# Kernel optimization log

Measured on AMD Instinct MI355X. Metric: run time of the kernel, lower is better.

Reference implementation:

```python
import jax, jax.numpy as jnp
import numpy as np

DIM = 768
H = 12
HEAD = DIM // H
SCALE = HEAD ** -0.5
NMM, NV, NA = 8, 4, 4


def _cross_attn(x1, x2, qw, kvw, pw, pb):
    # x1: [B,N1,C] queries, x2: [B,N2,C] keys/values. Weights stored [in,out].
    B, N1, C = x1.shape
    N2 = x2.shape[1]
    q = (x1 @ qw).reshape(B, N1, H, HEAD).transpose(0, 2, 1, 3)        # [B,H,N1,d]
    kv = (x2 @ kvw).reshape(B, N2, 2, H, HEAD)
    k = kv[:, :, 0].transpose(0, 2, 1, 3)                               # [B,H,N2,d]
    v = kv[:, :, 1].transpose(0, 2, 1, 3)
    attn = jax.nn.softmax(jnp.einsum('bhnd,bhmd->bhnm', q, k) * SCALE, axis=-1)
    o = jnp.einsum('bhnm,bhmd->bhnd', attn, v).transpose(0, 2, 1, 3).reshape(B, N1, C)
    return o @ pw + pb, attn


def setup_inputs() -> dict:
    key = jax.random.key(0)
    ks = jax.random.split(key, 16)
    s = 0.02
    inp = {
        'xmm': jax.random.normal(ks[0], (64, 16, DIM), jnp.float32),
        'xv': jax.random.normal(ks[1], (64, 784, DIM), jnp.float32),
        'xa': jax.random.normal(ks[2], (64, 512, DIM), jnp.float32),
        # visual cross-attn params (weights stored [in,out] = torch W.T)
        'qv_w': s * jax.random.normal(ks[3], (DIM, DIM), jnp.float32),
        'kvv_w': s * jax.random.normal(ks[4], (DIM, 2 * DIM), jnp.float32),
        'projv_w': s * jax.random.normal(ks[5], (DIM, DIM), jnp.float32),
        'projv_b': jnp.zeros((DIM,), jnp.float32),
        # audio cross-attn params
        'qa_w': s * jax.random.normal(ks[6], (DIM, DIM), jnp.float32),
        'kva_w': s * jax.random.normal(ks[7], (DIM, 2 * DIM), jnp.float32),
        'proja_w': s * jax.random.normal(ks[8], (DIM, DIM), jnp.float32),
        'proja_b': jnp.zeros((DIM,), jnp.float32),
        # factorized fusion attention params (dim_ratio=1.0 -> inner dim = DIM)
        'fq_w': s * jax.random.normal(ks[9], (DIM, DIM), jnp.float32),
        'fk_w': s * jax.random.normal(ks[10], (2 * DIM, DIM), jnp.float32),
        'fv_w': s * jax.random.normal(ks[11], (2 * DIM, DIM), jnp.float32),
        'fproj_w': s * jax.random.normal(ks[12], (DIM, DIM), jnp.float32),
        'fproj_b': jnp.zeros((DIM,), jnp.float32),
    }
    return inp


def reference(xmm, xv, xa, qv_w, kvv_w, projv_w, projv_b,
              qa_w, kva_w, proja_w, proja_b,
              fq_w, fk_w, fv_w, fproj_w, fproj_b):
    B = xmm.shape[0]
    xmm2 = xmm[:, :NMM]
    xmm_v, _ = _cross_attn(xmm[:, NMM:NMM + NV], xv, qv_w, kvv_w, projv_w, projv_b)
    xmm_a, _ = _cross_attn(xmm[:, NMM + NV:], xa, qa_w, kva_w, proja_w, proja_b)
    # outer-product token fusion: [B, NV*NA, 2*DIM]
    xva = jnp.concatenate([
        jnp.broadcast_to(xmm_v[:, :, None, :], (B, NV, NA, DIM)),
        jnp.broadcast_to(xmm_a[:, None, :, :], (B, NV, NA, DIM)),
    ], axis=-1).reshape(B, NV * NA, 2 * DIM)
    q = (xmm2 @ fq_w).reshape(B, NMM, H, -1).transpose(0, 2, 1, 3)
    k = (xva @ fk_w).reshape(B, NV * NA, H, -1).transpose(0, 2, 1, 3)
    v = (xva @ fv_w).reshape(B, NV * NA, H, -1).transpose(0, 2, 1, 3)
    attn = jax.nn.softmax(jnp.einsum('bhnd,bhmd->bhnm', q, k) * SCALE, axis=-1)
    o = jnp.einsum('bhnm,bhmd->bhnd', attn, v).transpose(0, 2, 1, 3).reshape(B, NMM, DIM)
    o = o @ fproj_w + fproj_b
    xmm_out = jnp.concatenate([o, xmm_v, xmm_a], axis=1)  # [B,16,DIM]
    return xmm_out, attn
```

## Files before the change

### kernel.cpp

```cpp
#include <hip/hip_runtime.h>
#include <stdint.h>

typedef unsigned short u16;
typedef unsigned int u32;
typedef __attribute__((ext_vector_type(8))) short short8;
typedef __attribute__((ext_vector_type(4))) float floatx4;


__device__ __forceinline__ u16 f2bf_rne(float f) {
  u32 u = __float_as_uint(f);
  return (u16)((u + 0x7fffu + ((u >> 16) & 1u)) >> 16);
}
__device__ __forceinline__ u32 pack_rne_u(u32 a, u32 b) {
  a += 0x7fffu + ((a >> 16) & 1u);
  b += 0x7fffu + ((b >> 16) & 1u);
  return __builtin_amdgcn_perm(b, a, 0x07060302u);
}
__device__ __forceinline__ void gld_lds16(const void* g, void* l) {
  __builtin_amdgcn_global_load_lds(
      (__attribute__((address_space(1))) void*)(uintptr_t)g,
      (__attribute__((address_space(3))) void*)l, 16, 0, 0);
}

__device__ __forceinline__ void block_sync_lds() {
  asm volatile("s_waitcnt lgkmcnt(0)" ::: "memory");
  __builtin_amdgcn_s_barrier();
  asm volatile("" ::: "memory");
}

__device__ __forceinline__ void sg_body(
    float (*sAt)[20], float (*sW)[64],
    const float* __restrict__ A, int a_pitch, int a_rb, int a_off,
    const float* __restrict__ W, const float* __restrict__ bias,
    float* __restrict__ Cout, int c_pitch, int c_rb, int c_off,
    int rt, int n0)
{
  const int t = threadIdx.x;
  const int g = t >> 6;
  const int c = t & 63;

  float acc[4] = {0.f, 0.f, 0.f, 0.f};

  for (int ks = 0; ks < 12; ++ks) {
    {
      int r = t >> 4;
      int c4 = (t & 15) * 4;
      int lr = rt * 16 + r;
      int grow = (lr / a_rb) * a_pitch + a_off + (lr % a_rb);
      float4 v = *(const float4*)(A + (size_t)grow * 768 + ks * 64 + c4);
      sAt[c4 + 0][r] = v.x;
      sAt[c4 + 1][r] = v.y;
      sAt[c4 + 2][r] = v.z;
      sAt[c4 + 3][r] = v.w;
    }
#pragma unroll
    for (int u = 0; u < 4; ++u) {
      int unit = t + u * 256;
      int r = unit >> 4;
      int c4 = (unit & 15) * 4;
      *(float4*)&sW[r][c4] = *(const float4*)(W + (size_t)(ks * 64 + r) * 768 + n0 + c4);
    }
    __syncthreads();
#pragma unroll 8
    for (int k = 0; k < 64; ++k) {
      float4 a4 = *(const float4*)&sAt[k][g * 4];
      float w = sW[k][c];
      acc[0] += a4.x * w;
      acc[1] += a4.y * w;
      acc[2] += a4.z * w;
      acc[3] += a4.w * w;
    }
    __syncthreads();
  }

  float bs = bias ? bias[n0 + c] : 0.f;
#pragma unroll
  for (int rr = 0; rr < 4; ++rr) {
    int lr = rt * 16 + g * 4 + rr;
    int grow = (lr / c_rb) * c_pitch + c_off + (lr % c_rb);
    Cout[(size_t)grow * 768 + n0 + c] = acc[rr] + bs;
  }
}

__global__ __launch_bounds__(256) void qproj(
    const float* __restrict__ xmm,
    const float* __restrict__ qv_w, const float* __restrict__ qa_w,
    const float* __restrict__ fq_w,
    float* __restrict__ q_v, float* __restrict__ q_a, float* __restrict__ q_f)
{
  __shared__ float sAt[64][20];
  __shared__ float sW[64][64];
  int rt = blockIdx.x;
  int n0 = blockIdx.y * 64;
  if (rt < 16)
    sg_body(sAt, sW, xmm, 16, 4, 8, qv_w, nullptr, q_v, 4, 4, 0, rt, n0);
  else if (rt < 32)
    sg_body(sAt, sW, xmm, 16, 4, 12, qa_w, nullptr, q_a, 4, 4, 0, rt - 16, n0);
  else
    sg_body(sAt, sW, xmm, 16, 8, 0, fq_w, nullptr, q_f, 8, 8, 0, rt - 32, n0);
}

__global__ __launch_bounds__(256) void proj2(
    const float* __restrict__ o_v, const float* __restrict__ o_a,
    const float* __restrict__ projv_w, const float* __restrict__ projv_b,
    const float* __restrict__ proja_w, const float* __restrict__ proja_b,
    float* __restrict__ out0)
{
  __shared__ float sAt[64][20];
  __shared__ float sW[64][64];
  int z = blockIdx.z;
  sg_body(sAt, sW, z ? o_a : o_v, 4, 4, 0,
          z ? proja_w : projv_w, z ? proja_b : projv_b,
          out0, 16, 4, z ? 12 : 8, blockIdx.x, blockIdx.y * 64);
}

__global__ __launch_bounds__(256) void fkv(
    const float* __restrict__ out0,
    const float* __restrict__ fk_w, const float* __restrict__ fv_w,
    float* __restrict__ kbase)
{
  __shared__ float sAt[64][20];
  __shared__ float sW[64][64];
  int z = blockIdx.z;
  const float* W = (z < 2) ? (fk_w + (size_t)(z & 1) * 768 * 768)
                           : (fv_w + (size_t)(z & 1) * 768 * 768);
  int a_off = (z & 1) ? 12 : 8;
  sg_body(sAt, sW, out0, 16, 4, a_off, W, nullptr,
          kbase + (size_t)z * 256 * 768, 4, 4, 0, blockIdx.x, blockIdx.y * 64);
}

__global__ __launch_bounds__(256) void fproj(
    const float* __restrict__ o_f,
    const float* __restrict__ fproj_w, const float* __restrict__ fproj_b,
    float* __restrict__ out0)
{
  __shared__ float sAt[64][20];
  __shared__ float sW[64][64];
  sg_body(sAt, sW, o_f, 8, 8, 0, fproj_w, fproj_b, out0, 16, 8, 0,
          blockIdx.x, blockIdx.y * 64);
}

__global__ __launch_bounds__(256) void qtilde(
    const float* __restrict__ q_v, const float* __restrict__ q_a,
    const float* __restrict__ kvv_w, const float* __restrict__ kva_w,
    u16* __restrict__ Qt_v, u16* __restrict__ Qt_a)
{
  __shared__ float sAt[64][20];
  __shared__ float sW[64][65];

  const int rt = blockIdx.x;
  const int nt = blockIdx.y;
  const int path = blockIdx.z / 12;
  const int h = blockIdx.z % 12;
  const float* q = path ? q_a : q_v;
  const float* kvw = path ? kva_w : kvv_w;
  u16* Qt = path ? Qt_a : Qt_v;

  const int t = threadIdx.x;
  const int g = t >> 6;
  const int c = t & 63;
  const int n0 = nt * 64;

  {
    int r = t >> 4;
    int c4 = (t & 15) * 4;
    float4 v = *(const float4*)(q + (size_t)(rt * 16 + r) * 768 + h * 64 + c4);
    sAt[c4 + 0][r] = v.x;
    sAt[c4 + 1][r] = v.y;
    sAt[c4 + 2][r] = v.z;
    sAt[c4 + 3][r] = v.w;
  }
#pragma unroll
  for (int u = 0; u < 4; ++u) {
    int unit = t + u * 256;
    int d = unit >> 4;
    int c4 = (unit & 15) * 4;
    float4 v = *(const float4*)(kvw + (size_t)(n0 + d) * 1536 + h * 64 + c4);
    sW[d][c4 + 0] = v.x;
    sW[d][c4 + 1] = v.y;
    sW[d][c4 + 2] = v.z;
    sW[d][c4 + 3] = v.w;
  }
  __syncthreads();

  float acc[4] = {0.f, 0.f, 0.f, 0.f};
#pragma unroll 16
  for (int e = 0; e < 64; ++e) {
    float4 a4 = *(const float4*)&sAt[e][g * 4];
    float w = sW[c][e];
    acc[0] += a4.x * w;
    acc[1] += a4.y * w;
    acc[2] += a4.z * w;
    acc[3] += a4.w * w;
  }
#pragma unroll
  for (int rr = 0; rr < 4; ++rr) {
    int rl = rt * 16 + g * 4 + rr;
    Qt[((size_t)(rl >> 2) * 48 + h * 4 + (rl & 3)) * 768 + n0 + c] = f2bf_rne(acc[rr]);
  }
}

__global__ __launch_bounds__(64) void attn_logits(
    const u16* __restrict__ Qt_v, const u16* __restrict__ Qt_a,
    const float* __restrict__ Xv, const float* __restrict__ Xa,
    float* __restrict__ Sv, float* __restrict__ Sa)
{
  const int bx = blockIdx.x;
  const int b = blockIdx.y;
  const int isA = (bx >= 49);
  const int T = isA ? (bx - 49) : bx;
  const u16* Qt = isA ? Qt_a : Qt_v;
  const float* X = isA ? Xa : Xv;
  float* S = isA ? Sa : Sv;
  const int N2 = isA ? 512 : 784;

  __shared__ __align__(16) u16 sX[16 * 768];

  const int lane = threadIdx.x;
  const int j0 = T * 16;
  const u32* Xt = (const u32*)(X + ((size_t)b * N2 + j0) * 768);
  const u16* Qb = Qt + (size_t)b * 48 * 768;
  const int ql = lane & 15;
  const int qs = lane >> 4;

  uint4 ra[6], rb[6];

#define L3_LOAD(buf, c_)                                                       \
  do {                                                                         \
    _Pragma("unroll") for (int i = 0; i < 6; ++i)                              \
      buf[i] = *(const uint4*)(Xt + (c_) * 1536 + i * 256 + lane * 4);         \
  } while (0)

#define L3_PACK(buf, c_)                                                       \
  do {                                                                         \
    _Pragma("unroll") for (int i = 0; i < 6; ++i) {                            \
      int jr_ = (c_) * 2 + i / 3;                                              \
      int colb_ = (i % 3) * 512 + lane * 8;                                    \
      uint2 w_;                                                                \
      w_.x = pack_rne_u(buf[i].x, buf[i].y);                                   \
      w_.y = pack_rne_u(buf[i].z, buf[i].w);                                   \
      *(uint2*)((char*)sX + jr_ * 1536 + (colb_ ^ ((jr_ & 7) << 4))) = w_;     \
    }                                                                          \
  } while (0)

  L3_LOAD(ra, 0);
#pragma unroll
  for (int c = 0; c < 8; ++c) {
    if (c + 1 < 8) {
      if (c & 1) L3_LOAD(ra, c + 1);
      else       L3_LOAD(rb, c + 1);
    }
    if (c & 1) L3_PACK(rb, c);
    else       L3_PACK(ra, c);
  }
#undef L3_LOAD
#undef L3_PACK
  asm volatile("s_waitcnt lgkmcnt(0)" ::: "memory");

  floatx4 acc[3];
#pragma unroll
  for (int i = 0; i < 3; ++i) acc[i] = (floatx4){0.f, 0.f, 0.f, 0.f};

#pragma unroll 4
  for (int kk = 0; kk < 24; ++kk) {
    short8 bf = *(const short8*)((char*)sX + ql * 1536 +
                                 ((kk * 64 + qs * 16) ^ ((ql & 7) << 4)));
#pragma unroll
    for (int i = 0; i < 3; ++i) {
      short8 qa = *(const short8*)(Qb + (size_t)(i * 16 + ql) * 768 +
                                   kk * 32 + qs * 8);
      acc[i] = __builtin_amdgcn_mfma_f32_16x16x32_bf16(qa, bf, acc[i], 0, 0, 0);
    }
  }

#pragma unroll
  for (int i = 0; i < 3; ++i)
#pragma unroll
    for (int r = 0; r < 4; ++r)
      S[((size_t)b * 48 + i * 16 + qs * 4 + r) * N2 + j0 + ql] =
          acc[i][r] * 0.125f;
}

__global__ __launch_bounds__(256) void softmax_p(
    const float* __restrict__ Sv, const float* __restrict__ Sa,
    u16* __restrict__ Pv, u16* __restrict__ Pa)
{
  const int z = blockIdx.z;
  const float* S = z ? Sa : Sv;
  u16* P = z ? Pa : Pv;
  const int N2 = z ? 512 : 784;
  const int N2p = z ? 512 : 832;

  const int hh = blockIdx.x;
  const int b = blockIdx.y;
  const int t = threadIdx.x;
  const int lane = t & 63;
  const int wave = t >> 6;
  const int row = hh * 4 + wave;
  const float* Srow = S + ((size_t)b * 48 + row) * N2;
  u16* Prow = P + ((size_t)b * 48 + row) * N2p;

  float m = -1e30f;
  for (int j = lane; j < N2; j += 64) m = fmaxf(m, Srow[j]);
#pragma unroll
  for (int off = 32; off > 0; off >>= 1) m = fmaxf(m, __shfl_xor(m, off));

  float e[13];
  float l = 0.f;
  int cnt = 0;
  for (int j = lane; j < N2; j += 64) {
    float p = __expf(Srow[j] - m);
    e[cnt++] = p;
    l += p;
  }
#pragma unroll
  for (int off = 32; off > 0; off >>= 1) l += __shfl_xor(l, off);
  float inv = 1.0f / l;

  cnt = 0;
  for (int j = lane; j < N2; j += 64) Prow[j] = f2bf_rne(e[cnt++] * inv);
  for (int j = N2 + lane; j < N2p; j += 64) Prow[j] = 0;
}

__global__ __launch_bounds__(256) void attn_px(
    const u16* __restrict__ Pv, const u16* __restrict__ Pa,
    const float* __restrict__ Xv, const float* __restrict__ Xa,
    float* __restrict__ Ov, float* __restrict__ Oa)
{
  const int z = blockIdx.z;
  const u16* P = z ? Pa : Pv;
  const float* X = z ? Xa : Xv;
  float* O = z ? Oa : Ov;
  const int N2 = z ? 512 : 784;
  const int N2p = z ? 512 : 832;

  __shared__ __align__(16) u16 sXT[2][128 * 72];

  const int t = threadIdx.x;
  const int lane = t & 63;
  const int wave = t >> 6;
  const int nt = blockIdx.x;
  const int b = blockIdx.y;
  const int n0 = nt * 128;
  const u16* Pb = P + (size_t)b * 48 * N2p;
  const float* Xb = X + (size_t)b * N2 * 768;
  const int Ks = N2p >> 6;

  const int jp0 = t >> 5;
  const int nq4 = (t & 31) * 4;
  const int qrow0 = lane & 15;
  const int qcb = (lane >> 4) * 8;

  floatx4 acc[3][2];
#pragma unroll
  for (int i = 0; i < 3; ++i)
#pragma unroll
    for (int j = 0; j < 2; ++j) acc[i][j] = (floatx4){0.f, 0.f, 0.f, 0.f};

  uint4 xA[4][2], xB[4][2];
  short8 qr[3][2];

#define PX_LOADX(dst, ks_)                                                     \
  do {                                                                         \
    _Pragma("unroll") for (int u = 0; u < 4; ++u) {                            \
      int j_ = (ks_) * 64 + (jp0 + u * 8) * 2;                                 \
      uint4 a0_ = {0u, 0u, 0u, 0u}, a1_ = {0u, 0u, 0u, 0u};                    \
      if (j_ < N2)                                                             \
        a0_ = *(const uint4*)(Xb + (size_t)j_ * 768 + n0 + nq4);               \
      if (j_ + 1 < N2)                                                         \
        a1_ = *(const uint4*)(Xb + (size_t)(j_ + 1) * 768 + n0 + nq4);         \
      dst[u][0] = a0_;                                                         \
      dst[u][1] = a1_;                                                         \
    }                                                                          \
  } while (0)

#define PX_LOADP(ks_)                                                          \
  do {                                                                         \
    _Pragma("unroll") for (int i = 0; i < 3; ++i)                              \
      _Pragma("unroll") for (int kk = 0; kk < 2; ++kk)                         \
        qr[i][kk] = *(const short8*)(Pb + (size_t)(i * 16 + qrow0) * N2p +     \
                                     (ks_) * 64 + kk * 32 + qcb);              \
  } while (0)

#define PX_WRITEX(src, bufp)                                                   \
  do {                                                                         \
    _Pragma("unroll") for (int u = 0; u < 4; ++u) {                            \
      int jl_ = (jp0 + u * 8) * 2;                                             \
      u32 w0_ = pack_rne_u(src[u][0].x, src[u][1].x);                          \
      u32 w1_ = pack_rne_u(src[u][0].y, src[u][1].y);                          \
      u32 w2_ = pack_rne_u(src[u][0].z, src[u][1].z);                          \
      u32 w3_ = pack_rne_u(src[u][0].w, src[u][1].w);                          \
      _Pragma("unroll") for (int m_ = 0; m_ < 4; ++m_) {                       \
        int n_ = nq4 + m_;                                                     \
        int sw_ = (((n_ >> 2) & 7) ^ ((n_ & 3) << 1)) * 8;                     \
        u32 wv_ = (m_ == 0) ? w0_ : (m_ == 1) ? w1_ : (m_ == 2) ? w2_ : w3_;   \
        *(u32*)((bufp) + n_ * 72 + (jl_ ^ sw_)) = wv_;                         \
      }                                                                        \
    }                                                                          \
  } while (0)

#define PX_COMPUTE(bufp)                                                       \
  do {                                                                         \
    _Pragma("unroll") for (int kk = 0; kk < 2; ++kk) {                         \
      _Pragma("unroll") for (int jj = 0; jj < 2; ++jj) {                       \
        int n_ = wave * 32 + jj * 16 + qrow0;                                  \
        int sw_ = (((n_ >> 2) & 7) ^ ((n_ & 3) << 1)) * 8;                     \
        int kb_ = kk * 32 + qcb;                                               \
        short8 bfr_ = *(const short8*)((bufp) + n_ * 72 + (kb_ ^ sw_));        \
        _Pragma("unroll") for (int i = 0; i < 3; ++i)                          \
          acc[i][jj] = __builtin_amdgcn_mfma_f32_16x16x32_bf16(                \
              qr[i][kk], bfr_, acc[i][jj], 0, 0, 0);                           \
      }                                                                        \
    }                                                                          \
  } while (0)

  u16* sT0 = &sXT[0][0];
  u16* sT1 = &sXT[1][0];

  PX_LOADX(xA, 0);
  PX_LOADP(0);
  int ks = 0;
  for (;;) {
    int more0 = (ks + 1 < Ks);
    if (more0) PX_LOADX(xB, ks + 1);
    PX_WRITEX(xA, sT0);
    block_sync_lds();
    PX_COMPUTE(sT0);
    if (!more0) break;
    PX_LOADP(ks + 1);
    ++ks;
    int more1 = (ks + 1 < Ks);
    if (more1) PX_LOADX(xA, ks + 1);
    PX_WRITEX(xB, sT1);
    block_sync_lds();
    PX_COMPUTE(sT1);
    if (!more1) break;
    PX_LOADP(ks + 1);
    ++ks;
  }
#undef PX_LOADX
#undef PX_LOADP
#undef PX_WRITEX
#undef PX_COMPUTE

  const int quad = lane >> 4;
  const int lc = lane & 15;
#pragma unroll
  for (int i = 0; i < 3; ++i)
#pragma unroll
    for (int jj = 0; jj < 2; ++jj) {
      int col = n0 + wave * 32 + jj * 16 + lc;
      int row0 = i * 16 + quad * 4;
#pragma unroll
      for (int r = 0; r < 4; ++r)
        O[((size_t)b * 48 + row0 + r) * 768 + col] = acc[i][jj][r];
    }
}

__global__ __launch_bounds__(256) void omix(
    const float* __restrict__ O_v, const float* __restrict__ O_a,
    const float* __restrict__ kvv_w, const float* __restrict__ kva_w,
    float* __restrict__ o_v, float* __restrict__ o_a)
{
  __shared__ float sAt[64][20];
  __shared__ float sW[64][64];

  const int z = blockIdx.z;
  const float* Ob = z ? O_a : O_v;
  const float* kvw = z ? kva_w : kvv_w;
  float* oo = z ? o_a : o_v;

  const int rt = blockIdx.x;
  const int h = blockIdx.y;
  const int t = threadIdx.x;
  const int g = t >> 6;
  const int c = t & 63;

  float acc[4] = {0.f, 0.f, 0.f, 0.f};

  for (int ks = 0; ks < 12; ++ks) {
    {
      int r = t >> 4;
      int c4 = (t & 15) * 4;
      int rl = rt * 16 + r;
      int arow = (rl >> 2) * 48 + h * 4 + (rl & 3);
      float4 v = *(const float4*)(Ob + (size_t)arow * 768 + ks * 64 + c4);
      sAt[c4 + 0][r] = v.x;
      sAt[c4 + 1][r] = v.y;
      sAt[c4 + 2][r] = v.z;
      sAt[c4 + 3][r] = v.w;
    }
#pragma unroll
    for (int u = 0; u < 4; ++u) {
      int unit = t + u * 256;
      int k = unit >> 4;
      int c4 = (unit & 15) * 4;
      *(float4*)&sW[k][c4] = *(const float4*)(kvw + (size_t)(ks * 64 + k) * 1536 + 768 + h * 64 + c4);
    }
    __syncthreads();
#pragma unroll 8
    for (int k = 0; k < 64; ++k) {
      float4 a4 = *(const float4*)&sAt[k][g * 4];
      float w = sW[k][c];
      acc[0] += a4.x * w;
      acc[1] += a4.y * w;
      acc[2] += a4.z * w;
      acc[3] += a4.w * w;
    }
    __syncthreads();
  }

#pragma unroll
  for (int rr = 0; rr < 4; ++rr) {
    int rl = rt * 16 + g * 4 + rr;
    oo[(size_t)rl * 768 + h * 64 + c] = acc[rr];
  }
}

__global__ __launch_bounds__(256) void fusion_attn(
    const float* __restrict__ Qf,
    const float* __restrict__ K1, const float* __restrict__ K2,
    const float* __restrict__ V1, const float* __restrict__ V2,
    float* __restrict__ Of,
    float* __restrict__ AttnOut)
{
  const int h = blockIdx.x;
  const int b = blockIdx.y;
  const int t = threadIdx.x;
  const int lane = t & 63;
  const int wave = t >> 6;

  __shared__ float sQ[8][64];
  __shared__ float sK1[4][64], sK2[4][64], sV1[4][64], sV2[4][64];
  __shared__ float sP[8][16];

  for (int idx = t; idx < 512; idx += 256)
    sQ[idx >> 6][idx & 63] = Qf[((size_t)(b * 8 + (idx >> 6))) * 768 + h * 64 + (idx & 63)];
  {
    size_t base = ((size_t)(b * 4 + wave)) * 768 + h * 64 + lane;
    sK1[wave][lane] = K1[base];
    sK2[wave][lane] = K2[base];
    sV1[wave][lane] = V1[base];
    sV2[wave][lane] = V2[base];
  }
  __syncthreads();

  if (t < 128) {
    int qi = t >> 4, m = t & 15, iv = m >> 2, ja = m & 3;
    float s = 0.f;
#pragma unroll
    for (int d = 0; d < 64; ++d) s += sQ[qi][d] * (sK1[iv][d] + sK2[ja][d]);
    s *= 0.125f;
    float mx = s;
#pragma unroll
    for (int off = 8; off > 0; off >>= 1) mx = fmaxf(mx, __shfl_xor(mx, off, 16));
    float p = __expf(s - mx);
    float l = p;
#pragma unroll
    for (int off = 8; off > 0; off >>= 1) l += __shfl_xor(l, off, 16);
    p = p / l;
    sP[qi][m] = p;
    AttnOut[(((size_t)b * 12 + h) * 8 + qi) * 16 + m] = p;
  }
  __syncthreads();

  for (int idx = t; idx < 512; idx += 256) {
    int qi = idx >> 6, d = idx & 63;
    float o = 0.f;
#pragma unroll
    for (int m = 0; m < 16; ++m) o += sP[qi][m] * (sV1[m >> 2][d] + sV2[m & 3][d]);
    Of[((size_t)(b * 8 + qi)) * 768 + h * 64 + d] = o;
  }
}

extern "C" void kernel_launch(void* const* d_in, const int* in_sizes, int n_in,
                              void* d_out, int out_size, void* d_ws, size_t ws_size,
                              hipStream_t stream)
{
  const float* xmm     = (const float*)d_in[0];
  const float* xv      = (const float*)d_in[1];
  const float* xa      = (const float*)d_in[2];
  const float* qv_w    = (const float*)d_in[3];
  const float* kvv_w   = (const float*)d_in[4];
  const float* projv_w = (const float*)d_in[5];
  const float* projv_b = (const float*)d_in[6];
  const float* qa_w    = (const float*)d_in[7];
  const float* kva_w   = (const float*)d_in[8];
  const float* proja_w = (const float*)d_in[9];
  const float* proja_b = (const float*)d_in[10];
  const float* fq_w    = (const float*)d_in[11];
  const float* fk_w    = (const float*)d_in[12];
  const float* fv_w    = (const float*)d_in[13];
  const float* fproj_w = (const float*)d_in[14];
  const float* fproj_b = (const float*)d_in[15];

  float* out0 = (float*)d_out;
  float* out1 = out0 + (size_t)64 * 16 * 768;

  char* ws = (char*)d_ws;
  size_t off = 0;
  float* q_v  = (float*)(ws + off); off += (size_t)256 * 768 * 4;
  float* q_a  = (float*)(ws + off); off += (size_t)256 * 768 * 4;
  float* q_f  = (float*)(ws + off); off += (size_t)512 * 768 * 4;
  u16*   Qt_v = (u16*)(ws + off);   off += (size_t)64 * 48 * 768 * 2;
  u16*   Qt_a = (u16*)(ws + off);   off += (size_t)64 * 48 * 768 * 2;
  float* S_v  = (float*)(ws + off); off += (size_t)64 * 48 * 784 * 4;
  float* S_a  = (float*)(ws + off); off += (size_t)64 * 48 * 512 * 4;
  u16*   P_v  = (u16*)(ws + off);   off += (size_t)64 * 48 * 832 * 2;
  u16*   P_a  = (u16*)(ws + off);   off += (size_t)64 * 48 * 512 * 2;
  float* O_v  = (float*)(ws + off); off += (size_t)64 * 48 * 768 * 4;
  float* O_a  = (float*)(ws + off); off += (size_t)64 * 48 * 768 * 4;
  float* o_v  = (float*)(ws + off); off += (size_t)256 * 768 * 4;
  float* o_a  = (float*)(ws + off); off += (size_t)256 * 768 * 4;
  float* kbase = (float*)(ws + off); off += (size_t)4 * 256 * 768 * 4;
  float* o_f  = (float*)(ws + off); off += (size_t)512 * 768 * 4;

  float* k1 = kbase;
  float* k2 = kbase + (size_t)256 * 768;
  float* v1 = kbase + (size_t)2 * 256 * 768;
  float* v2 = kbase + (size_t)3 * 256 * 768;

  qproj<<<dim3(64, 12), 256, 0, stream>>>(xmm, qv_w, qa_w, fq_w, q_v, q_a, q_f);
  qtilde<<<dim3(16, 12, 24), 256, 0, stream>>>(q_v, q_a, kvv_w, kva_w, Qt_v, Qt_a);
  attn_logits<<<dim3(81, 64), 64, 0, stream>>>(Qt_v, Qt_a, xv, xa, S_v, S_a);
  softmax_p<<<dim3(12, 64, 2), 256, 0, stream>>>(S_v, S_a, P_v, P_a);
  attn_px<<<dim3(6, 64, 2), 256, 0, stream>>>(P_v, P_a, xv, xa, O_v, O_a);
  omix<<<dim3(16, 12, 2), 256, 0, stream>>>(O_v, O_a, kvv_w, kva_w, o_v, o_a);
  proj2<<<dim3(16, 12, 2), 256, 0, stream>>>(o_v, o_a, projv_w, projv_b, proja_w, proja_b, out0);
  fkv<<<dim3(16, 12, 4), 256, 0, stream>>>(out0, fk_w, fv_w, kbase);
  fusion_attn<<<dim3(12, 64), 256, 0, stream>>>(q_f, k1, k2, v1, v2, o_f, out1);
  fproj<<<dim3(32, 12), 256, 0, stream>>>(o_f, fproj_w, fproj_b, out0);
}
```

Before: 618.2 us.

## Load X fragments directly into registers in attn_logits, 4-wave blocks

Rewrites the logits kernel to drop the LDS staging of the X tile: each lane loads its fp32 X fragment from global memory, packs it to bf16 in registers and feeds the MFMA directly. Blocks grow from one wave to four, each wave covering 32 key rows with two B fragments that share the Q fragments, and the grid is restructured to (7, 64, 2), with the audio half exiting early. This removes the LDS write/read round trip and improves Q reuse per load. In exchange each lane's X loads are strided by row rather than coalesced across the wave, and the tail rows are clamped and masked.

```diff
diff --git a/kernel.cpp b/kernel.cpp
--- a/kernel.cpp
+++ b/kernel.cpp
@@ -16,10 +16,13 @@
   b += 0x7fffu + ((b >> 16) & 1u);
   return __builtin_amdgcn_perm(b, a, 0x07060302u);
 }
-__device__ __forceinline__ void gld_lds16(const void* g, void* l) {
-  __builtin_amdgcn_global_load_lds(
-      (__attribute__((address_space(1))) void*)(uintptr_t)g,
-      (__attribute__((address_space(3))) void*)l, 16, 0, 0);
+__device__ __forceinline__ short8 pack8(uint4 a, uint4 b) {
+  union { u32 u[4]; short8 s; } cv;
+  cv.u[0] = pack_rne_u(a.x, a.y);
+  cv.u[1] = pack_rne_u(a.z, a.w);
+  cv.u[2] = pack_rne_u(b.x, b.y);
+  cv.u[3] = pack_rne_u(b.z, b.w);
+  return cv.s;
 }
 
 __device__ __forceinline__ void block_sync_lds() {
@@ -200,85 +203,79 @@
   }
 }
 
-__global__ __launch_bounds__(64) void attn_logits(
+__global__ __launch_bounds__(256) void attn_logits(
     const u16* __restrict__ Qt_v, const u16* __restrict__ Qt_a,
     const float* __restrict__ Xv, const float* __restrict__ Xa,
     float* __restrict__ Sv, float* __restrict__ Sa)
 {
-  const int bx = blockIdx.x;
+  const int z = blockIdx.z;
+  const int jt = blockIdx.x;
+  if (z == 1 && jt >= 4) return;
+  const u16* Qt = z ? Qt_a : Qt_v;
+  const float* X = z ? Xa : Xv;
+  float* S = z ? Sa : Sv;
+  const int N2 = z ? 512 : 784;
+
+  const int t = threadIdx.x;
+  const int lane = t & 63;
+  const int wave = t >> 6;
   const int b = blockIdx.y;
-  const int isA = (bx >= 49);
-  const int T = isA ? (bx - 49) : bx;
-  const u16* Qt = isA ? Qt_a : Qt_v;
-  const float* X = isA ? Xa : Xv;
-  float* S = isA ? Sa : Sv;
-  const int N2 = isA ? 512 : 784;
-
-  __shared__ __align__(16) u16 sX[16 * 768];
-
-  const int lane = threadIdx.x;
-  const int j0 = T * 16;
-  const u32* Xt = (const u32*)(X + ((size_t)b * N2 + j0) * 768);
+  const int j0 = jt * 128;
   const u16* Qb = Qt + (size_t)b * 48 * 768;
+  const float* Xb = X + (size_t)b * N2 * 768;
+
   const int ql = lane & 15;
   const int qs = lane >> 4;
 
-  uint4 ra[6], rb[6];
-
-#define L3_LOAD(buf, c_)                                                       \
-  do {                                                                         \
-    _Pragma("unroll") for (int i = 0; i < 6; ++i)                              \
-      buf[i] = *(const uint4*)(Xt + (c_) * 1536 + i * 256 + lane * 4);         \
-  } while (0)
-
-#define L3_PACK(buf, c_)                                                       \
-  do {                                                                         \
-    _Pragma("unroll") for (int i = 0; i < 6; ++i) {                            \
-      int jr_ = (c_) * 2 + i / 3;                                              \
-      int colb_ = (i % 3) * 512 + lane * 8;                                    \
-      uint2 w_;                                                                \
-      w_.x = pack_rne_u(buf[i].x, buf[i].y);                                   \
-      w_.y = pack_rne_u(buf[i].z, buf[i].w);                                   \
-      *(uint2*)((char*)sX + jr_ * 1536 + (colb_ ^ ((jr_ & 7) << 4))) = w_;     \
-    }                                                                          \
-  } while (0)
-
-  L3_LOAD(ra, 0);
-#pragma unroll
-  for (int c = 0; c < 8; ++c) {
-    if (c + 1 < 8) {
-      if (c & 1) L3_LOAD(ra, c + 1);
-      else       L3_LOAD(rb, c + 1);
-    }
-    if (c & 1) L3_PACK(rb, c);
-    else       L3_PACK(ra, c);
-  }
-#undef L3_LOAD
-#undef L3_PACK
-  asm volatile("s_waitcnt lgkmcnt(0)" ::: "memory");
-
-  floatx4 acc[3];
-#pragma unroll
-  for (int i = 0; i < 3; ++i) acc[i] = (floatx4){0.f, 0.f, 0.f, 0.f};
+  int row0 = j0 + wave * 32 + ql;
+  int row1 = row0 + 16;
+  if (row0 > N2 - 1) row0 = N2 - 1;
+  if (row1 > N2 - 1) row1 = N2 - 1;
+  const float* xP0 = Xb + (size_t)row0 * 768 + qs * 8;
+  const float* xP1 = Xb + (size_t)row1 * 768 + qs * 8;
+  const u16* qP0 = Qb + (size_t)(0 * 16 + ql) * 768 + qs * 8;
+  const u16* qP1 = Qb + (size_t)(1 * 16 + ql) * 768 + qs * 8;
+  const u16* qP2 = Qb + (size_t)(2 * 16 + ql) * 768 + qs * 8;
+
+  floatx4 acc[3][2];
+#pragma unroll
+  for (int i = 0; i < 3; ++i)
+#pragma unroll
+    for (int j = 0; j < 2; ++j) acc[i][j] = (floatx4){0.f, 0.f, 0.f, 0.f};
 
 #pragma unroll 4
   for (int kk = 0; kk < 24; ++kk) {
-    short8 bf = *(const short8*)((char*)sX + ql * 1536 +
-                                 ((kk * 64 + qs * 16) ^ ((ql & 7) << 4)));
-#pragma unroll
-    for (int i = 0; i < 3; ++i) {
-      short8 qa = *(const short8*)(Qb + (size_t)(i * 16 + ql) * 768 +
-                                   kk * 32 + qs * 8);
-      acc[i] = __builtin_amdgcn_mfma_f32_16x16x32_bf16(qa, bf, acc[i], 0, 0, 0);
-    }
-  }
-
+    uint4 x0a = *(const uint4*)(xP0 + kk * 32);
+    uint4 x0b = *(const uint4*)(xP0 + kk * 32 + 4);
+    uint4 x1a = *(const uint4*)(xP1 + kk * 32);
+    uint4 x1b = *(const uint4*)(xP1 + kk * 32 + 4);
+    short8 qa0 = *(const short8*)(qP0 + kk * 32);
+    short8 qa1 = *(const short8*)(qP1 + kk * 32);
+    short8 qa2 = *(const short8*)(qP2 + kk * 32);
+    short8 bf0 = pack8(x0a, x0b);
+    short8 bf1 = pack8(x1a, x1b);
+    acc[0][0] = __builtin_amdgcn_mfma_f32_16x16x32_bf16(qa0, bf0, acc[0][0], 0, 0, 0);
+    acc[0][1] = __builtin_amdgcn_mfma_f32_16x16x32_bf16(qa0, bf1, acc[0][1], 0, 0, 0);
+    acc[1][0] = __builtin_amdgcn_mfma_f32_16x16x32_bf16(qa1, bf0, acc[1][0], 0, 0, 0);
+    acc[1][1] = __builtin_amdgcn_mfma_f32_16x16x32_bf16(qa1, bf1, acc[1][1], 0, 0, 0);
+    acc[2][0] = __builtin_amdgcn_mfma_f32_16x16x32_bf16(qa2, bf0, acc[2][0], 0, 0, 0);
+    acc[2][1] = __builtin_amdgcn_mfma_f32_16x16x32_bf16(qa2, bf1, acc[2][1], 0, 0, 0);
+  }
+
+  const int quad = lane >> 4;
+  const int lc = lane & 15;
 #pragma unroll
   for (int i = 0; i < 3; ++i)
 #pragma unroll
-    for (int r = 0; r < 4; ++r)
-      S[((size_t)b * 48 + i * 16 + qs * 4 + r) * N2 + j0 + ql] =
-          acc[i][r] * 0.125f;
+    for (int jj = 0; jj < 2; ++jj) {
+      int col = j0 + wave * 32 + jj * 16 + lc;
+      if (col < N2) {
+        int row0s = i * 16 + quad * 4;
+#pragma unroll
+        for (int r = 0; r < 4; ++r)
+          S[((size_t)b * 48 + row0s + r) * N2 + col] = acc[i][jj][r] * 0.125f;
+      }
+    }
 }
 
 __global__ __launch_bounds__(256) void softmax_p(
@@ -622,7 +619,7 @@
 
   qproj<<<dim3(64, 12), 256, 0, stream>>>(xmm, qv_w, qa_w, fq_w, q_v, q_a, q_f);
   qtilde<<<dim3(16, 12, 24), 256, 0, stream>>>(q_v, q_a, kvv_w, kva_w, Qt_v, Qt_a);
-  attn_logits<<<dim3(81, 64), 64, 0, stream>>>(Qt_v, Qt_a, xv, xa, S_v, S_a);
+  attn_logits<<<dim3(7, 64, 2), 256, 0, stream>>>(Qt_v, Qt_a, xv, xa, S_v, S_a);
   softmax_p<<<dim3(12, 64, 2), 256, 0, stream>>>(S_v, S_a, P_v, P_a);
   attn_px<<<dim3(6, 64, 2), 256, 0, stream>>>(P_v, P_a, xv, xa, O_v, O_a);
   omix<<<dim3(16, 12, 2), 256, 0, stream>>>(O_v, O_a, kvv_w, kva_w, o_v, o_a);
```

After: 608.2 us. No clear change (-1.6%).
